# Kernel optimization log

Measured on AMD Instinct MI355X. Metric: run time of the kernel, lower is better.

The kernel has to match this reference:

```python
import jax, jax.numpy as jnp
import numpy as np

B, T, D_IN, H, N_LAYERS, D_OUT = 256, 512, 128, 512, 3, 1


def setup_inputs() -> dict:
    key = jax.random.key(0)
    ks = jax.random.split(key, 20)
    s = 1.0 / np.sqrt(H)
    inp = {"x": jax.random.normal(ks[0], (B, T, D_IN), dtype=jnp.float32)}
    k = 1
    for l in range(N_LAYERS):
        d_in = D_IN if l == 0 else H
        inp[f"W_ih_{l}"] = jax.random.uniform(ks[k], (4 * H, d_in), minval=-s, maxval=s); k += 1
        inp[f"W_hh_{l}"] = jax.random.uniform(ks[k], (4 * H, H), minval=-s, maxval=s); k += 1
        inp[f"b_ih_{l}"] = jax.random.uniform(ks[k], (4 * H,), minval=-s, maxval=s); k += 1
        inp[f"b_hh_{l}"] = jax.random.uniform(ks[k], (4 * H,), minval=-s, maxval=s); k += 1
    inp["W_fc"] = jax.random.uniform(ks[k], (D_OUT, H), minval=-s, maxval=s); k += 1
    inp["b_fc"] = jax.random.uniform(ks[k], (D_OUT,), minval=-s, maxval=s)
    return inp


def _lstm_layer(x, W_ih, W_hh, b_ih, b_hh):
    # x: [B, T, d_in] -> hs: [B, T, H]. PyTorch gate order: i, f, g, o.
    xg = jnp.einsum("btd,gd->btg", x, W_ih) + b_ih + b_hh  # precompute input proj [B,T,4H]
    Hh = W_hh.shape[1]
    Bb = x.shape[0]

    def step(carry, xg_t):
        h, c = carry
        g = xg_t + h @ W_hh.T  # [B, 4H]
        i, f, gg, o = jnp.split(g, 4, axis=-1)
        c = jax.nn.sigmoid(f) * c + jax.nn.sigmoid(i) * jnp.tanh(gg)
        h = jax.nn.sigmoid(o) * jnp.tanh(c)
        return (h, c), h

    h0 = jnp.zeros((Bb, Hh), x.dtype)
    (_, _), hs = jax.lax.scan(step, (h0, h0), jnp.swapaxes(xg, 0, 1))
    return jnp.swapaxes(hs, 0, 1)


def reference(x, W_ih_0, W_hh_0, b_ih_0, b_hh_0,
              W_ih_1, W_hh_1, b_ih_1, b_hh_1,
              W_ih_2, W_hh_2, b_ih_2, b_hh_2,
              W_fc, b_fc):
    # Eval mode: inter-layer dropout (p=0.4) is identity.
    h = _lstm_layer(x, W_ih_0, W_hh_0, b_ih_0, b_hh_0)
    h = _lstm_layer(h, W_ih_1, W_hh_1, b_ih_1, b_hh_1)
    h = _lstm_layer(h, W_ih_2, W_hh_2, b_ih_2, b_hh_2)
    return h[:, -1, :] @ W_fc.T + b_fc  # [B, D_OUT]
```

## Files before the change

### kernel.cpp

```cpp
#include <hip/hip_runtime.h>

#define B_   256
#define T_   512
#define DIN_ 128
#define H_   512
#define G4_  2048

typedef __bf16 bf16_t;
typedef __bf16 bf16x8 __attribute__((ext_vector_type(8)));
typedef __bf16 bf16x4 __attribute__((ext_vector_type(4)));
typedef float  f32x4  __attribute__((ext_vector_type(4)));
typedef float  f32x16 __attribute__((ext_vector_type(16)));

__device__ __forceinline__ void gload16cc(const void* g, void* l) {
  __builtin_amdgcn_global_load_lds(
      (const __attribute__((address_space(1))) unsigned int*)g,
      (__attribute__((address_space(3))) unsigned int*)l, 16, 0, 17);
}

__global__ void cast_f32_bf16(const float* __restrict__ s, bf16_t* __restrict__ d, int n) {
  int i = (blockIdx.x * 256 + threadIdx.x) * 4;
  if (i >= n) return;
  float4 v = *(const float4*)(s + i);
  bf16x4 o;
  o[0] = (bf16_t)v.x; o[1] = (bf16_t)v.y; o[2] = (bf16_t)v.z; o[3] = (bf16_t)v.w;
  *(bf16x4*)(d + i) = o;
}

__global__ void cast_strided(const float* __restrict__ s, bf16_t* __restrict__ d,
                             int Ks, int Kd, int coff) {
  int npr = Ks >> 3;
  int i = blockIdx.x * 256 + threadIdx.x;
  if (i >= 2048 * npr) return;
  int row = i / npr, j = i - row * npr;
  const float* sp = s + (size_t)row * Ks + j * 8;
  float4 v0 = *(const float4*)sp;
  float4 v1 = *(const float4*)(sp + 4);
  bf16x8 o;
  o[0] = (bf16_t)v0.x; o[1] = (bf16_t)v0.y; o[2] = (bf16_t)v0.z; o[3] = (bf16_t)v0.w;
  o[4] = (bf16_t)v1.x; o[5] = (bf16_t)v1.y; o[6] = (bf16_t)v1.z; o[7] = (bf16_t)v1.w;
  *(bf16x8*)(d + (size_t)row * Kd + coff + j * 8) = o;
}

__global__ void bias_sum(const float* __restrict__ a, const float* __restrict__ b,
                         float* __restrict__ o, int n) {
  int i = blockIdx.x * 256 + threadIdx.x;
  if (i < n) o[i] = a[i] + b[i];
}

#define RING_N (8 * 256 * 512)
#define FSTR   16

template<bool L0>
__device__ __forceinline__ void step_loop(
    char* smem, const bf16_t* __restrict__ xbf, const bf16_t* __restrict__ wcl,
    const float* __restrict__ bias_l, bf16_t* ringPrev, bf16_t* ringOwn,
    float* __restrict__ hsf, int* flags, int layer, int bg, int ug)
{
  constexpr int KL   = L0 ? 640 : 1024;
  constexpr int ROWB = KL * 2;
  constexpr int XT   = L0 ? 4 : 16;
  constexpr int HT   = 16;
  constexpr int NT   = XT + HT;
  constexpr int HOFF = L0 ? 256 : 1024;
  const int tid  = threadIdx.x;
  const int lane = tid & 63;
  const int wv   = tid >> 6;
  const int g    = wv & 3;
  const int kh   = wv >> 2;
  const int r32  = lane & 31;
  const int l5   = lane >> 5;
  const int u0   = ug * 32;
  const int t0x  = L0 ? (kh * 4) : (kh * 16);
  const int t0h  = L0 ? (8 + kh * 16) : (32 + kh * 16);

  bf16x8 wfrag[NT];
  {
    const bf16_t* wrow = wcl + (size_t)(g * 512 + u0 + r32) * KL + l5 * 8;
    #pragma unroll
    for (int i = 0; i < XT; ++i) wfrag[i]      = *(const bf16x8*)(wrow + (t0x + i) * 16);
    #pragma unroll
    for (int i = 0; i < HT; ++i) wfrag[XT + i] = *(const bf16x8*)(wrow + (t0h + i) * 16);
  }
  const int um = tid >> 3;
  const int uq = tid & 7;
  float bsv[4][4];
  #pragma unroll
  for (int g2 = 0; g2 < 4; ++g2)
    #pragma unroll
    for (int q = 0; q < 4; ++q)
      bsv[g2][q] = bias_l[g2 * 512 + u0 + uq * 4 + q];

  float cst[4] = {0.f, 0.f, 0.f, 0.f};
  float* gp = (float*)smem;

  int* fl_own  = flags + ((layer * 512) * 4 + bg) * FSTR;
  int* fl_prev = flags + (((layer - 1) * 512) * 4 + bg) * FSTR;
  int* fl_next = flags + (((layer + 1) * 512) * 4 + bg) * FSTR;

  for (int s = 0; s < 512; ++s) {
    const int slot  = s & 7;
    const int slot2 = (s - 1) & 7;
    if (!L0) {
      if (tid == 0)
        while (__hip_atomic_load(fl_prev + s * 4 * FSTR, __ATOMIC_RELAXED,
                                 __HIP_MEMORY_SCOPE_AGENT) < 16)
          __builtin_amdgcn_s_sleep(1);
      __syncthreads();
      const bf16_t* prvS = ringPrev + (size_t)slot * (256 * 512) + (size_t)(bg * 64) * 512;
      #pragma unroll
      for (int i = 0; i < 8; ++i) {
        int r = i * 8 + wv;
        gload16cc(prvS + r * 512 + (lane ^ (r & 15)) * 8, smem + r * ROWB);
      }
    } else {
      #pragma unroll
      for (int i2 = 0; i2 < 2; ++i2) {
        int idx = i2 * 512 + tid;
        int r = idx >> 4, cx = idx & 15;
        int px = cx ^ (r & 15);
        bf16x8 v = *(const bf16x8*)(xbf + ((size_t)(bg * 64 + r) * T_ + s) * 128 + cx * 8);
        *(bf16x8*)(smem + r * ROWB + px * 16) = v;
      }
    }
    __syncthreads();
    f32x16 acc0 = {}, acc1 = {};
    #pragma unroll
    for (int i = 0; i < XT; ++i) {
      const int px = ((t0x + i) * 2 + l5) ^ (r32 & 15);
      bf16x8 a0 = *(const bf16x8*)(smem + r32 * ROWB + px * 16);
      bf16x8 a1 = *(const bf16x8*)(smem + (32 + r32) * ROWB + px * 16);
      acc0 = __builtin_amdgcn_mfma_f32_32x32x16_bf16(a0, wfrag[i], acc0, 0, 0, 0);
      acc1 = __builtin_amdgcn_mfma_f32_32x32x16_bf16(a1, wfrag[i], acc1, 0, 0, 0);
    }
    if (tid == 0) {
      if (s > 0)
        while (__hip_atomic_load(fl_own + (s - 1) * 4 * FSTR, __ATOMIC_RELAXED,
                                 __HIP_MEMORY_SCOPE_AGENT) < 16)
          __builtin_amdgcn_s_sleep(1);
      if (layer < 2 && s >= 8)
        while (__hip_atomic_load(fl_next + (s - 8) * 4 * FSTR, __ATOMIC_RELAXED,
                                 __HIP_MEMORY_SCOPE_AGENT) < 16)
          __builtin_amdgcn_s_sleep(1);
    }
    __syncthreads();
    {
      const bf16_t* ownS = ringOwn + (size_t)slot2 * (256 * 512) + (size_t)(bg * 64) * 512;
      #pragma unroll
      for (int i = 0; i < 8; ++i) {
        int r = i * 8 + wv;
        gload16cc(ownS + r * 512 + (lane ^ (r & 15)) * 8, smem + r * ROWB + HOFF);
      }
    }
    __syncthreads();
    #pragma unroll
    for (int i = 0; i < HT; ++i) {
      const int px = ((t0h + i) * 2 + l5) ^ (r32 & 15);
      bf16x8 a0 = *(const bf16x8*)(smem + r32 * ROWB + px * 16);
      bf16x8 a1 = *(const bf16x8*)(smem + (32 + r32) * ROWB + px * 16);
      acc0 = __builtin_amdgcn_mfma_f32_32x32x16_bf16(a0, wfrag[XT + i], acc0, 0, 0, 0);
      acc1 = __builtin_amdgcn_mfma_f32_32x32x16_bf16(a1, wfrag[XT + i], acc1, 0, 0, 0);
    }
    __syncthreads();
    {
      const int base = kh * 8192 + g * 32 + r32;
      #pragma unroll
      for (int reg = 0; reg < 16; ++reg) {
        int mr = (reg & 3) + 8 * (reg >> 2) + 4 * l5;
        gp[base + mr * 128]        = acc0[reg];
        gp[base + (32 + mr) * 128] = acc1[reg];
      }
    }
    __syncthreads();
    union { bf16x4 v; unsigned long long u; } pk;
    f32x4 hvf;
    {
      f32x4 gv[4];
      #pragma unroll
      for (int g2 = 0; g2 < 4; ++g2) {
        f32x4 p0 = *(const f32x4*)&gp[um * 128 + g2 * 32 + uq * 4];
        f32x4 p1 = *(const f32x4*)&gp[8192 + um * 128 + g2 * 32 + uq * 4];
        #pragma unroll
        for (int q = 0; q < 4; ++q) gv[g2][q] = p0[q] + p1[q];
      }
      #pragma unroll
      for (int q = 0; q < 4; ++q) {
        float i_ = gv[0][q] + bsv[0][q];
        float f_ = gv[1][q] + bsv[1][q];
        float g_ = gv[2][q] + bsv[2][q];
        float o_ = gv[3][q] + bsv[3][q];
        float si = 1.f / (1.f + __expf(-i_));
        float sf = 1.f / (1.f + __expf(-f_));
        float so = 1.f / (1.f + __expf(-o_));
        float tg = 2.f / (1.f + __expf(-2.f * g_)) - 1.f;
        float cv = sf * cst[q] + si * tg;
        cst[q] = cv;
        float th = 2.f / (1.f + __expf(-2.f * cv)) - 1.f;
        hvf[q] = so * th;
        pk.v[q] = (bf16_t)hvf[q];
      }
    }
    {
      int b = bg * 64 + um;
      bf16_t* dst = ringOwn + (size_t)slot * (256 * 512) + (size_t)b * 512 + u0 + uq * 4;
      (void)__hip_atomic_exchange((unsigned long long*)dst, pk.u,
                                  __ATOMIC_RELAXED, __HIP_MEMORY_SCOPE_AGENT);
      if (layer == 2 && s == 511)
        *(f32x4*)(hsf + (size_t)b * 512 + u0 + uq * 4) = hvf;
    }
    __syncthreads();
    if (tid == 0)
      atomicAdd(fl_own + s * 4 * FSTR, 1);
  }
}

__global__ __launch_bounds__(512, 2)
void lstm_persist(const bf16_t* __restrict__ xbf, const bf16_t* __restrict__ wc,
                  const float* __restrict__ bias, bf16_t* __restrict__ rings,
                  float* __restrict__ hsf, int* __restrict__ flags)
{
  __shared__ __align__(16) char smem[131072];
  const int bid   = blockIdx.x;
  const int layer = bid >> 6;
  const int bg    = (bid >> 4) & 3;
  const int ug    = bid & 15;
  bf16_t* ringOwn  = rings + (size_t)layer * RING_N;
  bf16_t* ringPrev = rings + (size_t)(layer - 1) * RING_N;
  if (layer == 0) {
    step_loop<true>(smem, xbf, wc, bias, ringPrev, ringOwn, hsf, flags, 0, bg, ug);
  } else {
    const bf16_t* wcl = wc + 2048 * 640 + (size_t)(layer - 1) * 2048 * 1024;
    step_loop<false>(smem, xbf, wcl, bias + layer * 2048, ringPrev, ringOwn, hsf,
                     flags, layer, bg, ug);
  }
}

__global__ void fc_kernel(const float* __restrict__ h, const float* __restrict__ Wfc,
                          const float* __restrict__ bfc, float* __restrict__ out) {
  int b = blockIdx.x;
  int l = threadIdx.x;
  const float* hp = h + (size_t)b * H_;
  float acc = 0.f;
  #pragma unroll
  for (int i = 0; i < 8; ++i) acc += hp[l + i * 64] * Wfc[l + i * 64];
  #pragma unroll
  for (int off = 32; off; off >>= 1) acc += __shfl_down(acc, off, 64);
  if (l == 0) out[b] = acc + bfc[0];
}

extern "C" void kernel_launch(void* const* d_in, const int* in_sizes, int n_in,
                              void* d_out, int out_size, void* d_ws, size_t ws_size,
                              hipStream_t stream) {
  const float* x        = (const float*)d_in[0];
  const float* Wih_f[3] = {(const float*)d_in[1], (const float*)d_in[5], (const float*)d_in[9]};
  const float* Whh_f[3] = {(const float*)d_in[2], (const float*)d_in[6], (const float*)d_in[10]};
  const float* bih_f[3] = {(const float*)d_in[3], (const float*)d_in[7], (const float*)d_in[11]};
  const float* bhh_f[3] = {(const float*)d_in[4], (const float*)d_in[8], (const float*)d_in[12]};
  const float* Wfc = (const float*)d_in[13];
  const float* bfc = (const float*)d_in[14];

  char* ws = (char*)d_ws;
  size_t off = 0;
  auto take = [&](size_t bytes) { char* p = ws + off; off = (off + bytes + 255) & ~255ULL; return p; };
  bf16_t* XBF   = (bf16_t*)take((size_t)B_ * T_ * DIN_ * 2);
  bf16_t* WC    = (bf16_t*)take((size_t)(2048*640 + 2*2048*1024) * 2);
  float*  BIAS  = (float*) take(3 * 2048 * 4);
  bf16_t* RINGS = (bf16_t*)take((size_t)3 * RING_N * 2);
  float*  HSF   = (float*) take((size_t)B_ * H_ * 4);
  int*    FLAGS = (int*)   take(3 * 512 * 4 * FSTR * 4);

  bf16_t* WC1 = WC + 2048 * 640;
  bf16_t* WC2 = WC1 + 2048 * 1024;

  cast_f32_bf16<<<16384, 256, 0, stream>>>(x, XBF, B_ * T_ * DIN_);
  cast_strided<<<128, 256, 0, stream>>>(Wih_f[0], WC,  128, 640, 0);
  cast_strided<<<512, 256, 0, stream>>>(Whh_f[0], WC,  512, 640, 128);
  cast_strided<<<512, 256, 0, stream>>>(Wih_f[1], WC1, 512, 1024, 0);
  cast_strided<<<512, 256, 0, stream>>>(Whh_f[1], WC1, 512, 1024, 512);
  cast_strided<<<512, 256, 0, stream>>>(Wih_f[2], WC2, 512, 1024, 0);
  cast_strided<<<512, 256, 0, stream>>>(Whh_f[2], WC2, 512, 1024, 512);
  for (int l = 0; l < 3; ++l)
    bias_sum<<<8, 256, 0, stream>>>(bih_f[l], bhh_f[l], BIAS + l * 2048, G4_);
  hipMemsetAsync(RINGS, 0, (size_t)3 * RING_N * 2, stream);
  hipMemsetAsync(FLAGS, 0, 3 * 512 * 4 * FSTR * 4, stream);

  lstm_persist<<<192, 512, 0, stream>>>(XBF, WC, BIAS, RINGS, HSF, FLAGS);
  fc_kernel<<<B_, 64, 0, stream>>>(HSF, Wfc, bfc, (float*)d_out);
}
```

Baseline: 3.353 ms.

## Prefetch next-step input rows and split x-MFMAs to overlap own-h ring wait

Restructures the per-timestep schedule of the persistent LSTM kernel. The next step's input rows (x for layer 0, the previous layer's ring slot otherwise) are now loaded during the current step's gate computation instead of at the top of the next step. The input-projection MFMAs are split so half of them run after the own-hidden-state loads are issued, hiding that latency. The gate scratch buffer moves into the hidden-state region of shared memory, and several __syncthreads are replaced by raw s_barrier with explicit waitcnt. The hand-managed vmcnt/lgkmcnt ordering (including the per-wave vmcnt(1) exception) raises the risk of subtle races.

Result: slower. 4.740 ms (+41.4%).

```diff
diff --git a/kernel.cpp b/kernel.cpp
--- a/kernel.cpp
+++ b/kernel.cpp
@@ -17,6 +17,8 @@
       (const __attribute__((address_space(1))) unsigned int*)g,
       (__attribute__((address_space(3))) unsigned int*)l, 16, 0, 17);
 }
+
+#define SCHED_FENCE() __builtin_amdgcn_sched_barrier(0)
 
 __global__ void cast_f32_bf16(const float* __restrict__ s, bf16_t* __restrict__ d, int n) {
   int i = (blockIdx.x * 256 + threadIdx.x) * 4;
@@ -61,7 +63,7 @@
   constexpr int ROWB = KL * 2;
   constexpr int XT   = L0 ? 4 : 16;
   constexpr int HT   = 16;
-  constexpr int NT   = XT + HT;
+  constexpr int XP1  = L0 ? 2 : 8;
   constexpr int HOFF = L0 ? 256 : 1024;
   const int tid  = threadIdx.x;
   const int lane = tid & 63;
@@ -74,7 +76,7 @@
   const int t0x  = L0 ? (kh * 4) : (kh * 16);
   const int t0h  = L0 ? (8 + kh * 16) : (32 + kh * 16);
 
-  bf16x8 wfrag[NT];
+  bf16x8 wfrag[XT + HT];
   {
     const bf16_t* wrow = wcl + (size_t)(g * 512 + u0 + r32) * KL + l5 * 8;
     #pragma unroll
@@ -92,44 +94,49 @@
       bsv[g2][q] = bias_l[g2 * 512 + u0 + uq * 4 + q];
 
   float cst[4] = {0.f, 0.f, 0.f, 0.f};
-  float* gp = (float*)smem;
 
   int* fl_own  = flags + ((layer * 512) * 4 + bg) * FSTR;
   int* fl_prev = flags + (((layer - 1) * 512) * 4 + bg) * FSTR;
   int* fl_next = flags + (((layer + 1) * 512) * 4 + bg) * FSTR;
 
+  bf16x8 xv0 = {}, xv1 = {};
+
+  if (!L0) {
+    if (tid == 0)
+      while (__hip_atomic_load(fl_prev, __ATOMIC_RELAXED,
+                               __HIP_MEMORY_SCOPE_AGENT) < 16)
+        __builtin_amdgcn_s_sleep(1);
+    __builtin_amdgcn_s_barrier();
+    const bf16_t* prvS = ringPrev + (size_t)(bg * 64) * 512;
+    #pragma unroll
+    for (int i = 0; i < 8; ++i) {
+      int r = i * 8 + wv;
+      gload16cc(prvS + r * 512 + (lane ^ (r & 15)) * 8, smem + r * ROWB);
+    }
+    asm volatile("s_waitcnt vmcnt(0)" ::: "memory"); SCHED_FENCE();
+  } else {
+    #pragma unroll
+    for (int i2 = 0; i2 < 2; ++i2) {
+      int idx = i2 * 512 + tid, r = idx >> 4, cx = idx & 15;
+      bf16x8 v = *(const bf16x8*)(xbf + ((size_t)(bg * 64 + r) * T_ + 0) * 128 + cx * 8);
+      *(bf16x8*)(smem + r * ROWB + (cx ^ (r & 15)) * 16) = v;
+    }
+  }
+
   for (int s = 0; s < 512; ++s) {
     const int slot  = s & 7;
     const int slot2 = (s - 1) & 7;
-    if (!L0) {
-      if (tid == 0)
-        while (__hip_atomic_load(fl_prev + s * 4 * FSTR, __ATOMIC_RELAXED,
-                                 __HIP_MEMORY_SCOPE_AGENT) < 16)
-          __builtin_amdgcn_s_sleep(1);
-      __syncthreads();
-      const bf16_t* prvS = ringPrev + (size_t)slot * (256 * 512) + (size_t)(bg * 64) * 512;
-      #pragma unroll
-      for (int i = 0; i < 8; ++i) {
-        int r = i * 8 + wv;
-        gload16cc(prvS + r * 512 + (lane ^ (r & 15)) * 8, smem + r * ROWB);
-      }
-    } else {
-      #pragma unroll
-      for (int i2 = 0; i2 < 2; ++i2) {
-        int idx = i2 * 512 + tid;
-        int r = idx >> 4, cx = idx & 15;
-        int px = cx ^ (r & 15);
-        bf16x8 v = *(const bf16x8*)(xbf + ((size_t)(bg * 64 + r) * T_ + s) * 128 + cx * 8);
-        *(bf16x8*)(smem + r * ROWB + px * 16) = v;
-      }
-    }
-    __syncthreads();
+    if (wv == 0) { asm volatile("s_waitcnt vmcnt(1) lgkmcnt(0)" ::: "memory"); }
+    else         { asm volatile("s_waitcnt vmcnt(0) lgkmcnt(0)" ::: "memory"); }
+    SCHED_FENCE();
+    __builtin_amdgcn_s_barrier();
+
     f32x16 acc0 = {}, acc1 = {};
     #pragma unroll
-    for (int i = 0; i < XT; ++i) {
+    for (int i = 0; i < XP1; ++i) {
       const int px = ((t0x + i) * 2 + l5) ^ (r32 & 15);
-      bf16x8 a0 = *(const bf16x8*)(smem + r32 * ROWB + px * 16);
-      bf16x8 a1 = *(const bf16x8*)(smem + (32 + r32) * ROWB + px * 16);
+      bf16x8 a0 = *(const bf16x8*)(smem + (size_t)r32 * ROWB + px * 16);
+      bf16x8 a1 = *(const bf16x8*)(smem + (size_t)(32 + r32) * ROWB + px * 16);
       acc0 = __builtin_amdgcn_mfma_f32_32x32x16_bf16(a0, wfrag[i], acc0, 0, 0, 0);
       acc1 = __builtin_amdgcn_mfma_f32_32x32x16_bf16(a1, wfrag[i], acc1, 0, 0, 0);
     }
@@ -143,7 +150,7 @@
                                  __HIP_MEMORY_SCOPE_AGENT) < 16)
           __builtin_amdgcn_s_sleep(1);
     }
-    __syncthreads();
+    __builtin_amdgcn_s_barrier();
     {
       const bf16_t* ownS = ringOwn + (size_t)slot2 * (256 * 512) + (size_t)(bg * 64) * 512;
       #pragma unroll
@@ -152,34 +159,68 @@
         gload16cc(ownS + r * 512 + (lane ^ (r & 15)) * 8, smem + r * ROWB + HOFF);
       }
     }
+    #pragma unroll
+    for (int i = XP1; i < XT; ++i) {
+      const int px = ((t0x + i) * 2 + l5) ^ (r32 & 15);
+      bf16x8 a0 = *(const bf16x8*)(smem + (size_t)r32 * ROWB + px * 16);
+      bf16x8 a1 = *(const bf16x8*)(smem + (size_t)(32 + r32) * ROWB + px * 16);
+      acc0 = __builtin_amdgcn_mfma_f32_32x32x16_bf16(a0, wfrag[i], acc0, 0, 0, 0);
+      acc1 = __builtin_amdgcn_mfma_f32_32x32x16_bf16(a1, wfrag[i], acc1, 0, 0, 0);
+    }
     __syncthreads();
+    if (L0 && s + 1 < 512) {
+      int r0 = tid >> 4, c0 = tid & 15;
+      xv0 = *(const bf16x8*)(xbf + ((size_t)(bg * 64 + r0) * T_ + (s + 1)) * 128 + c0 * 8);
+      int i1 = 512 + tid, r1 = i1 >> 4, c1 = i1 & 15;
+      xv1 = *(const bf16x8*)(xbf + ((size_t)(bg * 64 + r1) * T_ + (s + 1)) * 128 + c1 * 8);
+    }
     #pragma unroll
     for (int i = 0; i < HT; ++i) {
       const int px = ((t0h + i) * 2 + l5) ^ (r32 & 15);
-      bf16x8 a0 = *(const bf16x8*)(smem + r32 * ROWB + px * 16);
-      bf16x8 a1 = *(const bf16x8*)(smem + (32 + r32) * ROWB + px * 16);
+      bf16x8 a0 = *(const bf16x8*)(smem + (size_t)r32 * ROWB + px * 16);
+      bf16x8 a1 = *(const bf16x8*)(smem + (size_t)(32 + r32) * ROWB + px * 16);
       acc0 = __builtin_amdgcn_mfma_f32_32x32x16_bf16(a0, wfrag[XT + i], acc0, 0, 0, 0);
       acc1 = __builtin_amdgcn_mfma_f32_32x32x16_bf16(a1, wfrag[XT + i], acc1, 0, 0, 0);
     }
-    __syncthreads();
+    if (!L0 && tid == 0 && s + 1 < 512)
+      while (__hip_atomic_load(fl_prev + (s + 1) * 4 * FSTR, __ATOMIC_RELAXED,
+                               __HIP_MEMORY_SCOPE_AGENT) < 16)
+        __builtin_amdgcn_s_sleep(1);
+    __builtin_amdgcn_s_barrier();
     {
-      const int base = kh * 8192 + g * 32 + r32;
+      char* pb = smem + HOFF + kh * 512 + (g * 32 + r32) * 4;
       #pragma unroll
       for (int reg = 0; reg < 16; ++reg) {
         int mr = (reg & 3) + 8 * (reg >> 2) + 4 * l5;
-        gp[base + mr * 128]        = acc0[reg];
-        gp[base + (32 + mr) * 128] = acc1[reg];
+        *(float*)(pb + (size_t)mr * ROWB)        = acc0[reg];
+        *(float*)(pb + (size_t)(32 + mr) * ROWB) = acc1[reg];
       }
     }
     __syncthreads();
+    if (s + 1 < 512) {
+      if (!L0) {
+        const bf16_t* prvS = ringPrev + (size_t)((s + 1) & 7) * (256 * 512) + (size_t)(bg * 64) * 512;
+        #pragma unroll
+        for (int i = 0; i < 8; ++i) {
+          int r = i * 8 + wv;
+          gload16cc(prvS + r * 512 + (lane ^ (r & 15)) * 8, smem + r * ROWB);
+        }
+      } else {
+        int r0 = tid >> 4, c0 = tid & 15;
+        *(bf16x8*)(smem + r0 * ROWB + (c0 ^ (r0 & 15)) * 16) = xv0;
+        int i1 = 512 + tid, r1 = i1 >> 4, c1 = i1 & 15;
+        *(bf16x8*)(smem + r1 * ROWB + (c1 ^ (r1 & 15)) * 16) = xv1;
+      }
+    }
     union { bf16x4 v; unsigned long long u; } pk;
     f32x4 hvf;
     {
+      const char* gpb = smem + (size_t)um * ROWB + HOFF;
       f32x4 gv[4];
       #pragma unroll
       for (int g2 = 0; g2 < 4; ++g2) {
-        f32x4 p0 = *(const f32x4*)&gp[um * 128 + g2 * 32 + uq * 4];
-        f32x4 p1 = *(const f32x4*)&gp[8192 + um * 128 + g2 * 32 + uq * 4];
+        f32x4 p0 = *(const f32x4*)(gpb + (g2 * 32 + uq * 4) * 4);
+        f32x4 p1 = *(const f32x4*)(gpb + 512 + (g2 * 32 + uq * 4) * 4);
         #pragma unroll
         for (int q = 0; q < 4; ++q) gv[g2][q] = p0[q] + p1[q];
       }
@@ -208,7 +249,8 @@
       if (layer == 2 && s == 511)
         *(f32x4*)(hsf + (size_t)b * 512 + u0 + uq * 4) = hvf;
     }
-    __syncthreads();
+    asm volatile("s_waitcnt vmcnt(0)" ::: "memory"); SCHED_FENCE();
+    __builtin_amdgcn_s_barrier();
     if (tid == 0)
       atomicAdd(fl_own + s * 4 * FSTR, 1);
   }
```
